# Kernel optimization log

Hardware: AMD Instinct MI355X
Metric: run time of the kernel (lower is better)

The kernel has to match this reference:

```python
import jax, jax.numpy as jnp
import numpy as np

D, P, R, F = 512, 64, 32, 256  # directions, points per ray, rank, virtual subcarriers


def setup_inputs() -> dict:
    key = jax.random.key(0)
    ks = jax.random.split(key, 6)
    return {
        "att_re": jax.random.normal(ks[0], (D, P, R), dtype=jnp.float32),
        "att_im": jax.random.normal(ks[1], (D, P, R), dtype=jnp.float32),
        "rad_re": jax.random.normal(ks[2], (D, P, R), dtype=jnp.float32),
        "rad_im": jax.random.normal(ks[3], (D, P, R), dtype=jnp.float32),
        "freq_re": jax.random.normal(ks[4], (F, R), dtype=jnp.float32),
        "freq_im": jax.random.normal(ks[5], (F, R), dtype=jnp.float32),
        "max_ray_length": 200,
    }


def reference(att_re, att_im, rad_re, rad_im, freq_re, freq_im, max_ray_length):
    att = (att_re + 1j * att_im).astype(jnp.complex64)   # (D,P,R)
    rad = (rad_re + 1j * rad_im).astype(jnp.complex64)   # (D,P,R)
    fv = (freq_re + 1j * freq_im).astype(jnp.complex64)  # (F,R)

    num_points = att.shape[1]
    num_dirs = att.shape[0]
    delta_t = jnp.asarray(max_ray_length / num_points, dtype=jnp.float32)

    # prefix-sum of conjugated attenuation along the ray (u_hat_rho)
    u_hat_rho = jnp.cumsum(att.conj() * delta_t, axis=1)  # (D,P,R)

    # Project each rank-R vector onto each frequency basis vector.
    # The original's v_outer / v_outer_outer einsums factor exactly into these dot products.
    a_proj = jnp.einsum('dpr,fr->dpf', att.conj(), fv)        # (D,P,F)
    r_proj = jnp.einsum('dpr,fr->dpf', rad.conj(), fv)        # (D,P,F)
    u_proj = jnp.einsum('dpr,fr->dpf', u_hat_rho.conj(), fv)  # (D,P,F)

    # first-order: sum over all points; second-order: points k >= 1 only
    first = jnp.sum(r_proj * a_proj, axis=(0, 1))                                   # (F,)
    second = jnp.sum(r_proj[:, 1:] * a_proj[:, 1:] * u_proj[:, 1:], axis=(0, 1))    # (F,)

    csi = (first + second) * delta_t / num_dirs  # (F,) complex64
    return csi
```

## Files before the change

### kernel.cpp

```cpp
#include <hip/hip_runtime.h>

#define ND 512
#define NP 64
#define NR 32
#define NF 256
#define RSTRIDE 56

typedef __attribute__((ext_vector_type(8))) short bf16x8;
typedef __attribute__((ext_vector_type(4))) float f32x4;

__device__ inline unsigned short f2bf(float x) {
    unsigned u = __builtin_bit_cast(unsigned, x);
    u += 0x7FFFu + ((u >> 16) & 1u);
    return (unsigned short)(u >> 16);
}
__device__ inline unsigned pack2(float a, float b) {
    return (unsigned)f2bf(a) | ((unsigned)f2bf(b) << 16);
}

__global__ __launch_bounds__(256, 2) void lrrt_mfma3_kernel(
    const float* __restrict__ att_re, const float* __restrict__ att_im,
    const float* __restrict__ rad_re, const float* __restrict__ rad_im,
    const float* __restrict__ freq_re, const float* __restrict__ freq_im,
    const int* __restrict__ mrl, float* __restrict__ out)
{
    __shared__ __align__(16) unsigned short s_mat[6][NP * RSTRIDE];
    __shared__ float s_segtot[256];

    const int t = threadIdx.x;
    const int d = blockIdx.x;
    const size_t base = (size_t)d * (NP * NR);
    const int lane = t & 63;
    const int wv = t >> 6;
    const int kg = lane >> 4;
    const int m_lo = lane & 15;

#pragma unroll
    for (int half = 0; half < 2; ++half) {
        const int w = t + half * 256;
        const int p = w >> 3;
        const int c = (w & 7) * 4;
        const size_t g = base + (size_t)p * NR + c;
        const int lo = p * RSTRIDE + c;
        float4 x;
        x = *(const float4*)(att_re + g);
        *(uint2*)&s_mat[0][lo] = make_uint2(pack2(x.x, x.y), pack2(x.z, x.w));
        x = *(const float4*)(att_im + g);
        *(uint2*)&s_mat[1][lo] = make_uint2(pack2(x.x, x.y), pack2(x.z, x.w));
        x = *(const float4*)(rad_re + g);
        *(uint2*)&s_mat[2][lo] = make_uint2(pack2(x.x, x.y), pack2(x.z, x.w));
        x = *(const float4*)(rad_im + g);
        *(uint2*)&s_mat[3][lo] = make_uint2(pack2(x.x, x.y), pack2(x.z, x.w));
    }

    const int cs_r = t & 31;
    const int cs_reim = (t >> 5) & 1;
    const int cs_seg = t >> 6;
    float vals[16];
    {
        const float* src = cs_reim ? att_im : att_re;
        float run = 0.f;
#pragma unroll
        for (int i = 0; i < 16; ++i) {
            run += src[base + (cs_seg * 16 + i) * NR + cs_r];
            vals[i] = run;
        }
        s_segtot[t] = run;
    }
    __syncthreads();

    {
        float off = 0.f;
#pragma unroll
        for (int s = 0; s < 3; ++s)
            if (s < cs_seg) off += s_segtot[s * 64 + cs_reim * 32 + cs_r];
        const float sgn = cs_reim ? -1.f : 1.f;
        unsigned short* dst = s_mat[4 + cs_reim];
#pragma unroll
        for (int i = 0; i < 16; ++i) {
            const int p = cs_seg * 16 + i;
            dst[p * RSTRIDE + cs_r] = (p == 0) ? (unsigned short)0
                                               : f2bf(sgn * (vals[i] + off));
        }
    }
    __syncthreads();

    bf16x8 bvr[4], bvi[4], bvn[4];
#pragma unroll
    for (int q = 0; q < 4; ++q) {
        const int n = 16 * (4 * wv + q) + m_lo;
        const float4* fre = (const float4*)(freq_re + (size_t)n * NR + 8 * kg);
        const float4* fim = (const float4*)(freq_im + (size_t)n * NR + 8 * kg);
        const float4 r0 = fre[0], r1 = fre[1];
        const float4 i0 = fim[0], i1 = fim[1];
        bf16x8 vr, vi, vn;
        vr[0] = f2bf(r0.x); vr[1] = f2bf(r0.y); vr[2] = f2bf(r0.z); vr[3] = f2bf(r0.w);
        vr[4] = f2bf(r1.x); vr[5] = f2bf(r1.y); vr[6] = f2bf(r1.z); vr[7] = f2bf(r1.w);
        vi[0] = f2bf(i0.x); vi[1] = f2bf(i0.y); vi[2] = f2bf(i0.z); vi[3] = f2bf(i0.w);
        vi[4] = f2bf(i1.x); vi[5] = f2bf(i1.y); vi[6] = f2bf(i1.z); vi[7] = f2bf(i1.w);
        vn[0] = f2bf(-r0.x); vn[1] = f2bf(-r0.y); vn[2] = f2bf(-r0.z); vn[3] = f2bf(-r0.w);
        vn[4] = f2bf(-r1.x); vn[5] = f2bf(-r1.y); vn[6] = f2bf(-r1.z); vn[7] = f2bf(-r1.w);
        bvr[q] = vr; bvi[q] = vi; bvn[q] = vn;
    }

    const float delta_t = (float)(*mrl) / (float)NP;
    float pre[4] = {0.f, 0.f, 0.f, 0.f};
    float pim[4] = {0.f, 0.f, 0.f, 0.f};
    const f32x4 zero = {0.f, 0.f, 0.f, 0.f};

#pragma unroll 1
    for (int mt = 0; mt < 4; ++mt) {
        const int off = (mt * 16 + m_lo) * RSTRIDE + 8 * kg;
        const bf16x8 a_r = *(const bf16x8*)&s_mat[0][off];
        const bf16x8 a_i = *(const bf16x8*)&s_mat[1][off];
        const bf16x8 r_r = *(const bf16x8*)&s_mat[2][off];
        const bf16x8 r_i = *(const bf16x8*)&s_mat[3][off];
        const bf16x8 c_r = *(const bf16x8*)&s_mat[4][off];
        const bf16x8 c_i = *(const bf16x8*)&s_mat[5][off];
#pragma unroll
        for (int q = 0; q < 4; ++q) {
            f32x4 Are = __builtin_amdgcn_mfma_f32_16x16x32_bf16(a_r, bvr[q], zero, 0, 0, 0);
            f32x4 Aim = __builtin_amdgcn_mfma_f32_16x16x32_bf16(a_r, bvi[q], zero, 0, 0, 0);
            f32x4 Bre = __builtin_amdgcn_mfma_f32_16x16x32_bf16(r_r, bvr[q], zero, 0, 0, 0);
            f32x4 Bim = __builtin_amdgcn_mfma_f32_16x16x32_bf16(r_r, bvi[q], zero, 0, 0, 0);
            f32x4 Ure = __builtin_amdgcn_mfma_f32_16x16x32_bf16(c_r, bvr[q], zero, 0, 0, 0);
            f32x4 Uim = __builtin_amdgcn_mfma_f32_16x16x32_bf16(c_r, bvi[q], zero, 0, 0, 0);
            Are = __builtin_amdgcn_mfma_f32_16x16x32_bf16(a_i, bvi[q], Are, 0, 0, 0);
            Aim = __builtin_amdgcn_mfma_f32_16x16x32_bf16(a_i, bvn[q], Aim, 0, 0, 0);
            Bre = __builtin_amdgcn_mfma_f32_16x16x32_bf16(r_i, bvi[q], Bre, 0, 0, 0);
            Bim = __builtin_amdgcn_mfma_f32_16x16x32_bf16(r_i, bvn[q], Bim, 0, 0, 0);
            Ure = __builtin_amdgcn_mfma_f32_16x16x32_bf16(c_i, bvi[q], Ure, 0, 0, 0);
            Uim = __builtin_amdgcn_mfma_f32_16x16x32_bf16(c_i, bvn[q], Uim, 0, 0, 0);
#pragma unroll
            for (int i = 0; i < 4; ++i) {
                const float qre = Bre[i] * Are[i] - Bim[i] * Aim[i];
                const float qim = Bre[i] * Aim[i] + Bim[i] * Are[i];
                const float cre = fmaf(delta_t, Ure[i], 1.0f);
                const float cim = delta_t * Uim[i];
                pre[q] = fmaf(qre, cre, fmaf(-qim, cim, pre[q]));
                pim[q] = fmaf(qim, cre, fmaf(qre, cim, pim[q]));
            }
        }
    }

    const float scale = delta_t / (float)ND;
#pragma unroll
    for (int q = 0; q < 4; ++q) {
        float re = pre[q], im = pim[q];
        re += __shfl_xor(re, 16, 64); im += __shfl_xor(im, 16, 64);
        re += __shfl_xor(re, 32, 64); im += __shfl_xor(im, 32, 64);
        if (lane < 16) {
            const int f = 16 * (4 * wv + q) + lane;
            atomicAdd(&out[f], re * scale);
            atomicAdd(&out[NF + f], im * scale);
        }
    }
}

extern "C" void kernel_launch(void* const* d_in, const int* in_sizes, int n_in,
                              void* d_out, int out_size, void* d_ws, size_t ws_size,
                              hipStream_t stream) {
    const float* att_re = (const float*)d_in[0];
    const float* att_im = (const float*)d_in[1];
    const float* rad_re = (const float*)d_in[2];
    const float* rad_im = (const float*)d_in[3];
    const float* freq_re = (const float*)d_in[4];
    const float* freq_im = (const float*)d_in[5];
    const int* mrl = (const int*)d_in[6];
    float* out = (float*)d_out;

    hipMemsetAsync(d_out, 0, (size_t)out_size * sizeof(float), stream);

    lrrt_mfma3_kernel<<<ND, 256, 0, stream>>>(
        att_re, att_im, rad_re, rad_im, freq_re, freq_im, mrl, out);
}
```

Measured before the change: 91.54 us.

## Replace global atomics with per-direction workspace partials and a reduction kernel

Each block now writes its per-frequency partial sums into its own slice of the workspace instead of doing atomicAdd on the output. A second small kernel sums the 512 partials per output element. This also removes the memset of the output. It avoids contention from 512 blocks atomically adding to the same 512 floats, at the cost of an extra kernel launch and about 1 MB of workspace traffic.

After: 86.60 us. -5.4%, faster.

```diff
diff --git a/kernel.cpp b/kernel.cpp
--- a/kernel.cpp
+++ b/kernel.cpp
@@ -22,7 +22,7 @@
     const float* __restrict__ att_re, const float* __restrict__ att_im,
     const float* __restrict__ rad_re, const float* __restrict__ rad_im,
     const float* __restrict__ freq_re, const float* __restrict__ freq_im,
-    const int* __restrict__ mrl, float* __restrict__ out)
+    const int* __restrict__ mrl, float* __restrict__ ws)
 {
     __shared__ __align__(16) unsigned short s_mat[6][NP * RSTRIDE];
     __shared__ float s_segtot[256];
@@ -144,6 +144,7 @@
     }
 
     const float scale = delta_t / (float)ND;
+    float* wsd = ws + (size_t)d * (2 * NF);
 #pragma unroll
     for (int q = 0; q < 4; ++q) {
         float re = pre[q], im = pim[q];
@@ -151,10 +152,32 @@
         re += __shfl_xor(re, 32, 64); im += __shfl_xor(im, 32, 64);
         if (lane < 16) {
             const int f = 16 * (4 * wv + q) + lane;
-            atomicAdd(&out[f], re * scale);
-            atomicAdd(&out[NF + f], im * scale);
+            wsd[f] = re * scale;
+            wsd[NF + f] = im * scale;
         }
     }
+}
+
+__global__ __launch_bounds__(256) void lrrt_reduce_kernel(
+    const float* __restrict__ ws, float* __restrict__ out)
+{
+    __shared__ float red[256];
+    const int jloc = threadIdx.x & 63;
+    const int dg = threadIdx.x >> 6;
+    const int j = blockIdx.x * 64 + jloc;
+    float s0 = 0.f, s1 = 0.f, s2 = 0.f, s3 = 0.f;
+    const int d0 = dg * 128;
+#pragma unroll 4
+    for (int dd = 0; dd < 128; dd += 4) {
+        s0 += ws[(size_t)(d0 + dd + 0) * (2 * NF) + j];
+        s1 += ws[(size_t)(d0 + dd + 1) * (2 * NF) + j];
+        s2 += ws[(size_t)(d0 + dd + 2) * (2 * NF) + j];
+        s3 += ws[(size_t)(d0 + dd + 3) * (2 * NF) + j];
+    }
+    red[threadIdx.x] = (s0 + s1) + (s2 + s3);
+    __syncthreads();
+    if (dg == 0)
+        out[j] = red[jloc] + red[64 + jloc] + red[128 + jloc] + red[192 + jloc];
 }
 
 extern "C" void kernel_launch(void* const* d_in, const int* in_sizes, int n_in,
@@ -168,9 +191,9 @@
     const float* freq_im = (const float*)d_in[5];
     const int* mrl = (const int*)d_in[6];
     float* out = (float*)d_out;
-
-    hipMemsetAsync(d_out, 0, (size_t)out_size * sizeof(float), stream);
+    float* ws = (float*)d_ws;
 
     lrrt_mfma3_kernel<<<ND, 256, 0, stream>>>(
-        att_re, att_im, rad_re, rad_im, freq_re, freq_im, mrl, out);
+        att_re, att_im, rad_re, rad_im, freq_re, freq_im, mrl, ws);
+    lrrt_reduce_kernel<<<8, 256, 0, stream>>>(ws, out);
 }
```
